# Kernel tuning notes

Hardware: AMD Instinct MI355X
Metric: run time of the kernel (lower is better)

The kernel has to match this reference:

```python
import jax, jax.numpy as jnp
import numpy as np

VOCAB, N_EMBD, BLOCK = 50257, 384, 2048
B, T = 4, 2048


def setup_inputs() -> dict:
    key = jax.random.key(0)
    ks = jax.random.split(key, 9)
    s = 0.02
    return {
        "idx": jax.random.randint(ks[0], (B, T), 0, VOCAB),
        "targets": jax.random.randint(ks[1], (B, T), 0, VOCAB),
        "tok_emb": jax.random.normal(ks[2], (VOCAB, N_EMBD), jnp.float32) * s,
        "pos_emb": jax.random.normal(ks[3], (BLOCK, N_EMBD), jnp.float32) * s,
        "Wk": jax.random.normal(ks[4], (N_EMBD, N_EMBD), jnp.float32) * s,  # stored (in,out)
        "Wq": jax.random.normal(ks[5], (N_EMBD, N_EMBD), jnp.float32) * s,
        "Wv": jax.random.normal(ks[6], (N_EMBD, N_EMBD), jnp.float32) * s,
        "W_head": jax.random.normal(ks[7], (N_EMBD, VOCAB), jnp.float32) * s,
        "b_head": jnp.zeros((VOCAB,), jnp.float32),
    }


def reference(idx, targets, tok_emb, pos_emb, Wk, Wq, Wv, W_head, b_head):
    Bb, Tt = idx.shape
    C = tok_emb.shape[1]
    x = tok_emb[idx] + pos_emb[:Tt]                      # [B,T,C]
    K = x @ Wk
    Q = x @ Wq
    V = x @ Wv
    scores = jnp.einsum('btc,bsc->bts', Q, K) / jnp.sqrt(jnp.float32(C))
    causal = jnp.tril(jnp.ones((Tt, Tt), dtype=bool))
    scores = jnp.where(causal, scores, -jnp.inf)
    weights = jax.nn.softmax(scores, axis=-1)
    out = jnp.einsum('bts,bsc->btc', weights, V)          # [B,T,C]
    logits = out @ W_head + b_head                        # [B,T,V]
    logits2d = logits.reshape(Bb * Tt, -1)
    tgt = targets.reshape(-1)
    logp = jax.nn.log_softmax(logits2d, axis=-1)
    loss = -jnp.mean(jnp.take_along_axis(logp, tgt[:, None], axis=1))
    return (logits2d, loss)
```

## Files before the change

### kernel.cpp

```cpp
#include <hip/hip_runtime.h>
#include <hip/hip_bf16.h>

#define AS1 __attribute__((address_space(1)))
#define AS3 __attribute__((address_space(3)))

typedef __bf16 bf16x8 __attribute__((ext_vector_type(8)));
typedef float  f32x4  __attribute__((ext_vector_type(4)));

__device__ __forceinline__ unsigned short f2b(float f) {
    union { __hip_bfloat16 h; unsigned short u; } v;
    v.h = __float2bfloat16(f);
    return v.u;
}

__device__ __forceinline__ void gload16(const void* g, void* l) {
    __builtin_amdgcn_global_load_lds((AS1 void*)(unsigned long long)g,
                                     (AS3 void*)(unsigned int)(unsigned long long)l,
                                     16, 0, 0);
}

__device__ __forceinline__ void gemm128_core(
    const char* Asrc, int ldaB,
    const char* Bsrc, int ldbB,
    int ksteps,
    unsigned short* lA, unsigned short* lB,
    f32x4 acc[4][4])
{
    const int tid  = threadIdx.x;
    const int wave = tid >> 6;
    const int lane = tid & 63;
    const int wm = wave >> 1, wn = wave & 1;

    const int srow = lane >> 2;
    const int skb  = (lane & 3) * 16;

    const char* a0 = Asrc + (size_t)(wave * 16 + srow) * ldaB + skb;
    const char* a1 = Asrc + (size_t)(64 + wave * 16 + srow) * ldaB + skb;
    const char* b0 = Bsrc + (size_t)(wave * 16 + srow) * ldbB + skb;
    const char* b1 = Bsrc + (size_t)(64 + wave * 16 + srow) * ldbB + skb;

    const int l15 = lane & 15, l4 = lane >> 4;

    gload16(a0, lA + wave * 512);
    gload16(a1, lA + 2048 + wave * 512);
    gload16(b0, lB + wave * 512);
    gload16(b1, lB + 2048 + wave * 512);
    a0 += 64; a1 += 64; b0 += 64; b1 += 64;
    __syncthreads();

    for (int ks = 0; ks < ksteps; ++ks) {
        const int cur = ks & 1;
        if (ks + 1 < ksteps) {
            unsigned short* sA = lA + (cur ^ 1) * 4096;
            unsigned short* sB = lB + (cur ^ 1) * 4096;
            gload16(a0, sA + wave * 512);
            gload16(a1, sA + 2048 + wave * 512);
            gload16(b0, sB + wave * 512);
            gload16(b1, sB + 2048 + wave * 512);
            a0 += 64; a1 += 64; b0 += 64; b1 += 64;
        }
        const unsigned short* rA = lA + cur * 4096;
        const unsigned short* rB = lB + cur * 4096;
        bf16x8 af[4], bg[4];
#pragma unroll
        for (int m = 0; m < 4; ++m)
            af[m] = *(const bf16x8*)(rA + (wm * 64 + m * 16 + l15) * 32 + l4 * 8);
#pragma unroll
        for (int n = 0; n < 4; ++n)
            bg[n] = *(const bf16x8*)(rB + (wn * 64 + n * 16 + l15) * 32 + l4 * 8);
#pragma unroll
        for (int m = 0; m < 4; ++m)
#pragma unroll
            for (int n = 0; n < 4; ++n)
                acc[m][n] = __builtin_amdgcn_mfma_f32_16x16x32_bf16(af[m], bg[n], acc[m][n], 0, 0, 0);
        __syncthreads();
    }
}

__global__ __launch_bounds__(384) void k_embed(
    const int* __restrict__ idx, const float* __restrict__ tok,
    const float* __restrict__ pos, unsigned short* __restrict__ xb)
{
    const int i = blockIdx.x;
    const int c = threadIdx.x;
    const int t = i & 2047;
    float v = tok[(size_t)idx[i] * 384 + c] + pos[(size_t)t * 384 + c];
    xb[(size_t)i * 384 + c] = f2b(v);
}

__global__ __launch_bounds__(256) void k_wt_all(
    const float* __restrict__ Wq, const float* __restrict__ Wk,
    const float* __restrict__ Wv, unsigned short* __restrict__ wt)
{
    int gid = blockIdx.x * 256 + threadIdx.x;
    if (gid >= 1152 * 384) return;
    int n = gid / 384, k = gid % 384;
    const float* W; int col;
    if (n < 384)      { W = Wq; col = n; }
    else if (n < 768) { W = Wk; col = n - 384; }
    else              { W = Wv; col = n - 768; }
    wt[gid] = f2b(W[(size_t)k * 384 + col]);
}

__global__ __launch_bounds__(256) void k_wht(
    const float* __restrict__ Wh, unsigned short* __restrict__ wht)
{
    __shared__ unsigned short tile[32][33];
    const int n0 = blockIdx.x * 32, k0 = blockIdx.y * 32;
    const int tx = threadIdx.x, ty = threadIdx.y;
#pragma unroll
    for (int yy = ty; yy < 32; yy += 8) {
        int n = n0 + tx;
        float v = (n < 50257) ? Wh[(size_t)(k0 + yy) * 50257 + n] : 0.f;
        tile[yy][tx] = f2b(v);
    }
    __syncthreads();
#pragma unroll
    for (int yy = ty; yy < 32; yy += 8)
        wht[(size_t)(n0 + yy) * 384 + k0 + tx] = tile[tx][yy];
}

__global__ __launch_bounds__(256) void k_vt(
    const unsigned short* __restrict__ qkv, unsigned short* __restrict__ vt)
{
    __shared__ unsigned short tile[32][33];
    const int t0 = blockIdx.x * 32, c0 = blockIdx.y * 32, b = blockIdx.z;
    const int tx = threadIdx.x, ty = threadIdx.y;
#pragma unroll
    for (int yy = ty; yy < 32; yy += 8)
        tile[yy][tx] = qkv[((size_t)b * 2048 + t0 + yy) * 1152 + 768 + c0 + tx];
    __syncthreads();
#pragma unroll
    for (int yy = ty; yy < 32; yy += 8)
        vt[((size_t)b * 384 + c0 + yy) * 2048 + t0 + tx] = tile[tx][yy];
}

__global__ __launch_bounds__(256) void k_gemm_qkv(
    const unsigned short* __restrict__ xb, const unsigned short* __restrict__ wt,
    unsigned short* __restrict__ qkv)
{
    __shared__ unsigned short lA[8192], lB[8192];
    const int brow = blockIdx.x * 128;
    const int bcol = blockIdx.y * 128;
    f32x4 acc[4][4] = {};
    gemm128_core((const char*)(xb + (size_t)brow * 384), 768,
                 (const char*)(wt + (size_t)bcol * 384), 768, 12, lA, lB, acc);
    const int tid = threadIdx.x, wave = tid >> 6, lane = tid & 63;
    const int wm = wave >> 1, wn = wave & 1, l15 = lane & 15, l4 = lane >> 4;
#pragma unroll
    for (int m = 0; m < 4; ++m)
#pragma unroll
        for (int n = 0; n < 4; ++n)
#pragma unroll
            for (int r = 0; r < 4; ++r) {
                int row = brow + wm * 64 + m * 16 + l4 * 4 + r;
                int col = bcol + wn * 64 + n * 16 + l15;
                qkv[(size_t)row * 1152 + col] = f2b(acc[m][n][r]);
            }
}

__global__ __launch_bounds__(256) void k_gemm_scores(
    const unsigned short* __restrict__ qkv, float* __restrict__ scores)
{
    const int j = blockIdx.x, i = blockIdx.y, b = blockIdx.z;
    if (j > i) return;
    __shared__ unsigned short lA[8192], lB[8192];
    f32x4 acc[4][4] = {};
    const unsigned short* Q = qkv + ((size_t)b * 2048 + i * 128) * 1152;
    const unsigned short* K = qkv + ((size_t)b * 2048 + j * 128) * 1152 + 384;
    gemm128_core((const char*)Q, 2304, (const char*)K, 2304, 12, lA, lB, acc);
    const int tid = threadIdx.x, wave = tid >> 6, lane = tid & 63;
    const int wm = wave >> 1, wn = wave & 1, l15 = lane & 15, l4 = lane >> 4;
    const float sc = 0.0510310363f;
#pragma unroll
    for (int m = 0; m < 4; ++m)
#pragma unroll
        for (int n = 0; n < 4; ++n)
#pragma unroll
            for (int r = 0; r < 4; ++r) {
                int t = i * 128 + wm * 64 + m * 16 + l4 * 4 + r;
                int s = j * 128 + wn * 64 + n * 16 + l15;
                float v = (s <= t) ? acc[m][n][r] * sc : -1e30f;
                scores[((size_t)b * 2048 + t) * 2048 + s] = v;
            }
}

__global__ __launch_bounds__(256) void k_softmax(float* __restrict__ scores)
{
    const int row = blockIdx.x;
    const int t = row & 2047;
    const int Send = ((t >> 7) + 1) << 7;
    const int tid = threadIdx.x, lane = tid & 63, wave = tid >> 6;
    float* srow = scores + (size_t)row * 2048;
    unsigned short* wrow = (unsigned short*)scores + (size_t)row * 4096;

    float vals[8]; int cnt = 0;
    float sum = 0.f;
    for (int s = tid; s < Send; s += 256) {
        float e = __expf(srow[s]);
        vals[cnt++] = e; sum += e;
    }
    __shared__ float red[4];
#pragma unroll
    for (int off = 32; off; off >>= 1) sum += __shfl_xor(sum, off);
    if (lane == 0) red[wave] = sum;
    __syncthreads();
    sum = red[0] + red[1] + red[2] + red[3];

    float inv = 1.f / sum;
    int k2 = 0;
    for (int s = tid; s < Send; s += 256) wrow[s] = f2b(vals[k2++] * inv);
}

__global__ __launch_bounds__(256) void k_gemm_pv(
    const float* __restrict__ scores, const unsigned short* __restrict__ vt,
    unsigned short* __restrict__ outb)
{
    const int x = blockIdx.x;
    const int i = blockIdx.y;
    const int b = blockIdx.z;
    __shared__ unsigned short lA[8192], lB[8192];
    f32x4 acc[4][4] = {};
    const unsigned short* A = (const unsigned short*)scores + ((size_t)b * 2048 + i * 128) * 4096;
    const unsigned short* B = vt + ((size_t)b * 384 + x * 128) * 2048;
    gemm128_core((const char*)A, 8192, (const char*)B, 4096, (i + 1) * 4, lA, lB, acc);
    const int tid = threadIdx.x, wave = tid >> 6, lane = tid & 63;
    const int wm = wave >> 1, wn = wave & 1, l15 = lane & 15, l4 = lane >> 4;
#pragma unroll
    for (int m = 0; m < 4; ++m)
#pragma unroll
        for (int n = 0; n < 4; ++n)
#pragma unroll
            for (int r = 0; r < 4; ++r) {
                int row = b * 2048 + i * 128 + wm * 64 + m * 16 + l4 * 4 + r;
                int col = x * 128 + wn * 64 + n * 16 + l15;
                outb[(size_t)row * 384 + col] = f2b(acc[m][n][r]);
            }
}

__global__ __launch_bounds__(256) void k_gemm_head(
    const unsigned short* __restrict__ outb, const unsigned short* __restrict__ wht,
    const float* __restrict__ bhead, float* __restrict__ logits,
    float* __restrict__ ps)
{
    const int i = blockIdx.x;
    const int jn = blockIdx.y;
    const int brow = i * 128, bcol = jn * 128;
    __shared__ unsigned short lA[8192], lB[8192];
    __shared__ float part[128][33];
    f32x4 acc[4][4] = {};
    gemm128_core((const char*)(outb + (size_t)brow * 384), 768,
                 (const char*)(wht + (size_t)bcol * 384), 768, 12, lA, lB, acc);
    const int tid = threadIdx.x, wave = tid >> 6, lane = tid & 63;
    const int wm = wave >> 1, wn = wave & 1, l15 = lane & 15, l4 = lane >> 4;

    float bv[4]; int cv[4]; bool ok[4];
#pragma unroll
    for (int n = 0; n < 4; ++n) {
        int c = bcol + wn * 64 + n * 16 + l15;
        cv[n] = c;
        ok[n] = (c < 50257);
        bv[n] = ok[n] ? bhead[c] : 0.f;
    }
#pragma unroll
    for (int m = 0; m < 4; ++m) {
#pragma unroll
        for (int r = 0; r < 4; ++r) {
            int rloc = wm * 64 + m * 16 + l4 * 4 + r;
            size_t grow = (size_t)(brow + rloc);
            float s = 0.f;
#pragma unroll
            for (int n = 0; n < 4; ++n) {
                float x = acc[m][n][r] + bv[n];
                if (ok[n]) {
                    logits[grow * 50257 + cv[n]] = x;
                    s += __expf(x);
                }
            }
            part[rloc][wn * 16 + l15] = s;
        }
    }
    __syncthreads();
    if (tid < 128) {
        float S = 0.f;
#pragma unroll 8
        for (int j = 0; j < 32; ++j) S += part[tid][j];
        ps[(size_t)(brow + tid) * 393 + jn] = S;
    }
}

__global__ __launch_bounds__(256) void k_loss_row(
    const float* __restrict__ ps, const float* __restrict__ logits,
    const int* __restrict__ targets, float* __restrict__ rowloss)
{
    const int tid = threadIdx.x;
    const int row = blockIdx.x * 4 + (tid >> 6);
    const int lane = tid & 63;
    float s = 0.f;
    for (int nb = lane; nb < 393; nb += 64) s += ps[(size_t)row * 393 + nb];
#pragma unroll
    for (int off = 32; off; off >>= 1) s += __shfl_xor(s, off);
    if (lane == 0) {
        float lse = logf(s);
        int tg = targets[row];
        float lt = logits[(size_t)row * 50257 + tg];
        rowloss[row] = lse - lt;
    }
}

__global__ __launch_bounds__(256) void k_loss_final(
    const float* __restrict__ rowloss, float* __restrict__ out_loss)
{
    const int tid = threadIdx.x;
    float s = 0.f;
    for (int r = tid; r < 8192; r += 256) s += rowloss[r];
    __shared__ float red2[256];
    red2[tid] = s;
    __syncthreads();
    for (int off = 128; off; off >>= 1) {
        if (tid < off) red2[tid] += red2[tid + off];
        __syncthreads();
    }
    if (tid == 0) out_loss[0] = red2[0] * (1.0f / 8192.0f);
}

extern "C" void kernel_launch(void* const* d_in, const int* in_sizes, int n_in,
                              void* d_out, int out_size, void* d_ws, size_t ws_size,
                              hipStream_t stream)
{
    (void)in_sizes; (void)n_in; (void)out_size; (void)ws_size;
    const int*   idx = (const int*)d_in[0];
    const int*   tgt = (const int*)d_in[1];
    const float* tok = (const float*)d_in[2];
    const float* pos = (const float*)d_in[3];
    const float* Wk  = (const float*)d_in[4];
    const float* Wq  = (const float*)d_in[5];
    const float* Wv  = (const float*)d_in[6];
    const float* Wh  = (const float*)d_in[7];
    const float* bh  = (const float*)d_in[8];

    float* logits = (float*)d_out;
    float* loss   = logits + (size_t)8192 * 50257;

    char* ws = (char*)d_ws;
    unsigned short* xb   = (unsigned short*)(ws + 0);
    unsigned short* wt   = (unsigned short*)(ws + 6291456);
    unsigned short* qkv  = (unsigned short*)(ws + 7176192);
    unsigned short* vt   = (unsigned short*)(ws + 26050560);
    unsigned short* outb = (unsigned short*)(ws + 32342016);
    unsigned short* wht  = (unsigned short*)(ws + 38633472);
    float* scores        = (float*)(ws + 77266944);
    float* psb           = (float*)(ws + 144375808);
    float* rl            = (float*)(ws + 157253632);

    k_embed      <<<dim3(8192),       dim3(384),   0, stream>>>(idx, tok, pos, xb);
    k_wt_all     <<<dim3(1728),       dim3(256),   0, stream>>>(Wq, Wk, Wv, wt);
    k_wht        <<<dim3(1572, 12),   dim3(32, 8), 0, stream>>>(Wh, wht);
    k_gemm_qkv   <<<dim3(64, 9),      dim3(256),   0, stream>>>(xb, wt, qkv);
    k_vt         <<<dim3(64, 12, 4),  dim3(32, 8), 0, stream>>>(qkv, vt);
    k_gemm_scores<<<dim3(16, 16, 4),  dim3(256),   0, stream>>>(qkv, scores);
    k_softmax    <<<dim3(8192),       dim3(256),   0, stream>>>(scores);
    k_gemm_pv    <<<dim3(3, 16, 4),   dim3(256),   0, stream>>>(scores, vt, outb);
    k_gemm_head  <<<dim3(64, 393),    dim3(256),   0, stream>>>(outb, wht, bh, logits, psb);
    k_loss_row   <<<dim3(2048),       dim3(256),   0, stream>>>(psb, logits, tgt, rl);
    k_loss_final <<<dim3(1),          dim3(256),   0, stream>>>(rl, loss);
}
```

Baseline: 1.132 ms.

## Rework GEMM core LDS layout, fine-grained waits, and XCD-aware head block mapping

Changes the shared GEMM core so each wave stages contiguous 16-row chunks that match the MFMA fragment layout, letting fragment reads be lane-contiguous. The single barrier per step is replaced by an explicit vmcnt wait that keeps the next stage's loads in flight, plus barriers fenced with sched_barrier. The head GEMM launch is flattened to a 1D grid and remapped so consecutive blocks on the same XCD share row tiles, aiming to improve L2 reuse. The manual waitcnt accounting and the id remap risk subtle correctness or ordering problems if the load counts differ from the assumptions.

```diff
diff --git a/kernel.cpp b/kernel.cpp
--- a/kernel.cpp
+++ b/kernel.cpp
@@ -31,50 +31,58 @@
     const int lane = tid & 63;
     const int wm = wave >> 1, wn = wave & 1;
 
-    const int srow = lane >> 2;
-    const int skb  = (lane & 3) * 16;
-
-    const char* a0 = Asrc + (size_t)(wave * 16 + srow) * ldaB + skb;
-    const char* a1 = Asrc + (size_t)(64 + wave * 16 + srow) * ldaB + skb;
-    const char* b0 = Bsrc + (size_t)(wave * 16 + srow) * ldbB + skb;
-    const char* b1 = Bsrc + (size_t)(64 + wave * 16 + srow) * ldbB + skb;
-
-    const int l15 = lane & 15, l4 = lane >> 4;
-
-    gload16(a0, lA + wave * 512);
-    gload16(a1, lA + 2048 + wave * 512);
-    gload16(b0, lB + wave * 512);
-    gload16(b1, lB + 2048 + wave * 512);
-    a0 += 64; a1 += 64; b0 += 64; b1 += 64;
-    __syncthreads();
+    const int c0 = 2 * wave, c1 = 2 * wave + 1;
+    const int srowl = lane & 15;
+    const int skb   = (lane >> 4) * 16;
+
+    const char* a0 = Asrc + (size_t)(c0 * 16 + srowl) * ldaB + skb;
+    const char* a1 = Asrc + (size_t)(c1 * 16 + srowl) * ldaB + skb;
+    const char* b0 = Bsrc + (size_t)(c0 * 16 + srowl) * ldbB + skb;
+    const char* b1 = Bsrc + (size_t)(c1 * 16 + srowl) * ldbB + skb;
+
+#define STAGE(BOFF) do { \
+        gload16(a0, lA + (BOFF) + c0 * 512); \
+        gload16(a1, lA + (BOFF) + c1 * 512); \
+        gload16(b0, lB + (BOFF) + c0 * 512); \
+        gload16(b1, lB + (BOFF) + c1 * 512); \
+        a0 += 64; a1 += 64; b0 += 64; b1 += 64; } while (0)
+
+    STAGE(0);
 
     for (int ks = 0; ks < ksteps; ++ks) {
         const int cur = ks & 1;
         if (ks + 1 < ksteps) {
-            unsigned short* sA = lA + (cur ^ 1) * 4096;
-            unsigned short* sB = lB + (cur ^ 1) * 4096;
-            gload16(a0, sA + wave * 512);
-            gload16(a1, sA + 2048 + wave * 512);
-            gload16(b0, sB + wave * 512);
-            gload16(b1, sB + 2048 + wave * 512);
-            a0 += 64; a1 += 64; b0 += 64; b1 += 64;
+            STAGE((cur ^ 1) * 4096);
+            asm volatile("s_waitcnt vmcnt(4)" ::: "memory");
+        } else {
+            asm volatile("s_waitcnt vmcnt(0)" ::: "memory");
         }
+        __builtin_amdgcn_sched_barrier(0);
+        __builtin_amdgcn_s_barrier();
+        __builtin_amdgcn_sched_barrier(0);
+        asm volatile("" ::: "memory");
+
         const unsigned short* rA = lA + cur * 4096;
         const unsigned short* rB = lB + cur * 4096;
         bf16x8 af[4], bg[4];
 #pragma unroll
         for (int m = 0; m < 4; ++m)
-            af[m] = *(const bf16x8*)(rA + (wm * 64 + m * 16 + l15) * 32 + l4 * 8);
+            af[m] = *(const bf16x8*)(rA + (wm * 4 + m) * 512 + lane * 8);
 #pragma unroll
         for (int n = 0; n < 4; ++n)
-            bg[n] = *(const bf16x8*)(rB + (wn * 64 + n * 16 + l15) * 32 + l4 * 8);
+            bg[n] = *(const bf16x8*)(rB + (wn * 4 + n) * 512 + lane * 8);
 #pragma unroll
         for (int m = 0; m < 4; ++m)
 #pragma unroll
             for (int n = 0; n < 4; ++n)
                 acc[m][n] = __builtin_amdgcn_mfma_f32_16x16x32_bf16(af[m], bg[n], acc[m][n], 0, 0, 0);
-        __syncthreads();
-    }
+
+        __builtin_amdgcn_sched_barrier(0);
+        asm volatile("" ::: "memory");
+        __builtin_amdgcn_s_barrier();
+        __builtin_amdgcn_sched_barrier(0);
+    }
+#undef STAGE
 }
 
 __global__ __launch_bounds__(384) void k_embed(
@@ -243,8 +251,10 @@
     const float* __restrict__ bhead, float* __restrict__ logits,
     float* __restrict__ ps)
 {
-    const int i = blockIdx.x;
-    const int jn = blockIdx.y;
+    const int id  = blockIdx.x;
+    const int sid = (id & 7) * 3144 + (id >> 3);
+    const int i  = sid & 63;
+    const int jn = sid >> 6;
     const int brow = i * 128, bcol = jn * 128;
     __shared__ unsigned short lA[8192], lB[8192];
     __shared__ float part[128][33];
@@ -361,7 +371,7 @@
     k_gemm_scores<<<dim3(16, 16, 4),  dim3(256),   0, stream>>>(qkv, scores);
     k_softmax    <<<dim3(8192),       dim3(256),   0, stream>>>(scores);
     k_gemm_pv    <<<dim3(3, 16, 4),   dim3(256),   0, stream>>>(scores, vt, outb);
-    k_gemm_head  <<<dim3(64, 393),    dim3(256),   0, stream>>>(outb, wht, bh, logits, psb);
+    k_gemm_head  <<<dim3(25152),      dim3(256),   0, stream>>>(outb, wht, bh, logits, psb);
     k_loss_row   <<<dim3(2048),       dim3(256),   0, stream>>>(psb, logits, tgt, rl);
     k_loss_final <<<dim3(1),          dim3(256),   0, stream>>>(rl, loss);
 }
```

Result: slower. 1.383 ms (+22.1%).
